# Kernel tuning notes

Measured on AMD Instinct MI355X. Metric: run time of the kernel, lower is better.

The kernel has to match this reference:

```python
import jax, jax.numpy as jnp
import numpy as np

D_MODEL = 1024
NUM_HEADS = 16

def _dense_params(key, d_in, d_out):
    kw, _ = jax.random.split(key)
    # flax default: lecun_normal kernel, zeros bias
    W = jax.random.normal(kw, (d_in, d_out), dtype=jnp.float32) / np.sqrt(d_in)
    b = jnp.zeros((d_out,), dtype=jnp.float32)
    return W, b

def setup_inputs() -> dict:
    key = jax.random.key(0)
    ks = jax.random.split(key, 8)
    B, Tx, Tc = 2, 2048, 2048
    x = jax.random.normal(ks[0], (B, Tx, D_MODEL), dtype=jnp.float32)
    context = jax.random.normal(ks[1], (B, Tc, D_MODEL), dtype=jnp.float32)
    Wq, bq = _dense_params(ks[2], D_MODEL, D_MODEL)
    Wks, bks = _dense_params(ks[3], D_MODEL, D_MODEL)
    Wvs, bvs = _dense_params(ks[4], D_MODEL, D_MODEL)
    Wkc, bkc = _dense_params(ks[5], D_MODEL, D_MODEL)
    Wvc, bvc = _dense_params(ks[6], D_MODEL, D_MODEL)
    Wo, bo = _dense_params(ks[7], D_MODEL, D_MODEL)
    return {"x": x, "context": context,
            "Wq": Wq, "bq": bq, "Wks": Wks, "bks": bks, "Wvs": Wvs, "bvs": bvs,
            "Wkc": Wkc, "bkc": bkc, "Wvc": Wvc, "bvc": bvc, "Wo": Wo, "bo": bo}

def _split_heads(t, H):
    B, T, C = t.shape
    return t.reshape(B, T, H, C // H).transpose(0, 2, 1, 3)  # [B,H,T,hd]

def reference(x, context, Wq, bq, Wks, bks, Wvs, bvs, Wkc, bkc, Wvc, bvc, Wo, bo):
    H = NUM_HEADS
    head_dim = D_MODEL // H
    q = x @ Wq + bq
    k = jnp.concatenate([x @ Wks + bks, context @ Wkc + bkc], axis=1)
    v = jnp.concatenate([x @ Wvs + bvs, context @ Wvc + bvc], axis=1)
    q = _split_heads(q, H)  # [B,H,Tq,hd]
    k = _split_heads(k, H)  # [B,H,Tk,hd]
    v = _split_heads(v, H)
    attn = jnp.einsum('bhqd,bhkd->bhqk', q, k) / jnp.sqrt(jnp.float32(head_dim))
    attn = jax.nn.softmax(attn, axis=-1)
    out = jnp.einsum('bhqk,bhkd->bhqd', attn, v)
    B, _, Tq, _ = out.shape
    out = out.transpose(0, 2, 1, 3).reshape(B, Tq, D_MODEL)
    return out @ Wo + bo
```

## Files before the change

### kernel.cpp

```cpp
#include <hip/hip_runtime.h>
#include <hip/hip_bf16.h>
#include <math.h>


typedef _Float16 f16;
typedef _Float16 f16x8 __attribute__((ext_vector_type(8)));
typedef _Float16 f16x4v __attribute__((ext_vector_type(4)));
typedef _Float16 f16x2 __attribute__((ext_vector_type(2)));
typedef float    f32x4 __attribute__((ext_vector_type(4)));
typedef float    f32x16 __attribute__((ext_vector_type(16)));
typedef unsigned u32x4v __attribute__((ext_vector_type(4)));

#define MFMA_F16(a, b, c)  __builtin_amdgcn_mfma_f32_16x16x32_f16((a), (b), (c), 0, 0, 0)
#define MFMA32_F16(a, b, c) __builtin_amdgcn_mfma_f32_32x32x16_f16((a), (b), (c), 0, 0, 0)

#define QSCALE 0.18033688011112042f

__device__ __forceinline__ void glds16(const f16* g, f16* l) {
    __builtin_amdgcn_global_load_lds(
        (const __attribute__((address_space(1))) void*)g,
        (__attribute__((address_space(3))) void*)l, 16, 0, 0);
}

__device__ __forceinline__ unsigned pk16(float a, float b) {
    f16x2 t = { (f16)a, (f16)b };
    return __builtin_bit_cast(unsigned, t);
}

__global__ __launch_bounds__(256) void prep(
    const float4* __restrict__ x, const float4* __restrict__ ctx,
    f16x4v* __restrict__ xb, f16x4v* __restrict__ cb,
    const float* __restrict__ W0, const float* __restrict__ W1,
    const float* __restrict__ W2, const float* __restrict__ W3,
    const float* __restrict__ W4, const float* __restrict__ W5,
    f16* __restrict__ wt)
{
    if (blockIdx.x < 8192) {
        const int n4 = (2 * 2048 * 1024) / 4;
        int i = blockIdx.x * 256 + threadIdx.x;
        float4 v;
        f16x4v* dst;
        if (i < n4) { v = x[i];        dst = xb + i; }
        else        { v = ctx[i - n4]; dst = cb + (i - n4); }
        f16x4v h = { (f16)v.x, (f16)v.y, (f16)v.z, (f16)v.w };
        *dst = h;
        return;
    }
    const int idx = blockIdx.x - 8192;
    const int z = idx >> 10, rem = idx & 1023;
    const float* Ws[6] = { W0, W1, W2, W3, W4, W5 };
    const float* W = Ws[z];
    f16* Wt = wt + (size_t)z * (1024 * 1024);

    __shared__ float tile[32][33];
    const int tx = threadIdx.x & 31, ty = threadIdx.x >> 5;
    const int n0 = (rem & 31) * 32, k0 = (rem >> 5) * 32;

#pragma unroll
    for (int i = 0; i < 4; ++i) {
        int r = i * 8 + ty;
        tile[r][tx] = W[(size_t)(k0 + r) * 1024 + n0 + tx];
    }
    __syncthreads();
#pragma unroll
    for (int i = 0; i < 4; ++i) {
        int r = i * 8 + ty;
        Wt[(size_t)(n0 + r) * 1024 + k0 + tx] = (f16)tile[tx][r];
    }
}

#define GEMM_PROLOGUE(BN)                                                     \
    const int m0 = blockIdx.x * 128, n0 = blockIdx.y * (BN);                  \
    const int tid = threadIdx.x;                                              \
    const int w = tid >> 6, lane = tid & 63, quad = lane >> 4, l15 = lane & 15;\
    const int wm = (w >> 1) * 64, wn = (w & 1) * ((BN) / 2);                  \
    const int qsw = (quad ^ ((l15 >> 1) & 3)) * 8;                            \
    int gA[2], gB[(BN) / 64];                                                 \
    _Pragma("unroll")                                                         \
    for (int p = 0; p < 2; ++p) {                                             \
        int s = tid + p * 256;                                                \
        int r = (s >> 2) & 127, c = (s & 3) ^ ((s >> 3) & 3);                 \
        gA[p] = (m0 + r) * 1024 + c * 8;                                      \
    }                                                                         \
    _Pragma("unroll")                                                         \
    for (int p = 0; p < (BN) / 64; ++p) {                                     \
        int s = tid + p * 256;                                                \
        int r = (s >> 2) & ((BN) - 1), c = (s & 3) ^ ((s >> 3) & 3);          \
        gB[p] = (n0 + r) * 1024 + c * 8;                                      \
    }

#define GEMM_STAGE_TO(BN, buf, koff)                                          \
    _Pragma("unroll")                                                         \
    for (int p = 0; p < 2; ++p)                                               \
        glds16(&A[gA[p] + (koff)], &As[buf][(p * 256 + w * 64) * 8]);         \
    _Pragma("unroll")                                                         \
    for (int p = 0; p < (BN) / 64; ++p)                                       \
        glds16(&Bt[gB[p] + (koff)], &Bs[buf][(p * 256 + w * 64) * 8]);

__global__ __launch_bounds__(256) void proj_gemm(
    const f16* __restrict__ xb, const f16* __restrict__ cb,
    const f16* __restrict__ wt,
    const float* __restrict__ bq, const float* __restrict__ bks,
    const float* __restrict__ bkc, const float* __restrict__ bvs,
    const float* __restrict__ bvc,
    f16* __restrict__ qbuf, f16* __restrict__ kbuf, f16* __restrict__ vbuf)
{
    __shared__ alignas(16) f16 As[2][128 * 32];
    __shared__ alignas(16) f16 Bs[2][128 * 32];

    const int z = blockIdx.z;
    const f16* A = (z == 0 || z == 1 || z == 3) ? xb : cb;
    const int wslot = (z == 0) ? 0 : (z == 1) ? 1 : (z == 2) ? 3 : (z == 3) ? 2 : 4;
    const f16* Bt = wt + (size_t)wslot * 1048576;
    const float* bias = (z == 0) ? bq : (z == 1) ? bks : (z == 2) ? bkc
                        : (z == 3) ? bvs : bvc;
    const int roff = (z == 2 || z == 4) ? 2048 : 0;

    GEMM_PROLOGUE(128)
    f32x4 acc[4][4] = {};

    GEMM_STAGE_TO(128, 0, 0)

    for (int k0 = 0; k0 < 1024; k0 += 32) {
        const int cur = (k0 >> 5) & 1;
        __syncthreads();
        if (k0 + 32 < 1024) {
            GEMM_STAGE_TO(128, cur ^ 1, k0 + 32)
        }
        f16x8 a[4], b[4];
#pragma unroll
        for (int i = 0; i < 4; ++i)
            a[i] = *(const f16x8*)&As[cur][(wm + i * 16 + l15) * 32 + qsw];
#pragma unroll
        for (int i = 0; i < 4; ++i)
            b[i] = *(const f16x8*)&Bs[cur][(wn + i * 16 + l15) * 32 + qsw];
#pragma unroll
        for (int mi = 0; mi < 4; ++mi)
#pragma unroll
            for (int ni = 0; ni < 4; ++ni)
                acc[mi][ni] = MFMA_F16(a[mi], b[ni], acc[mi][ni]);
    }

#pragma unroll
    for (int mi = 0; mi < 4; ++mi) {
#pragma unroll
        for (int r = 0; r < 4; ++r) {
            int row = m0 + wm + mi * 16 + quad * 4 + r;
            int b_ = row >> 11, tok = row & 2047;
#pragma unroll
            for (int ni = 0; ni < 4; ++ni) {
                int col = n0 + wn + ni * 16 + l15;
                float v = acc[mi][ni][r] + bias[col];
                int bh = b_ * 16 + (col >> 6);
                int tg = roff + tok;
                if (z == 0) {
                    qbuf[((size_t)bh * 2048 + tok) * 64 + (col & 63)] = (f16)(v * QSCALE);
                } else if (z <= 2) {
                    kbuf[(size_t)bh * 262144 + (size_t)(tg >> 6) * 4096
                         + (size_t)((col >> 5) & 1) * 2048 + (tg & 63) * 32 + (col & 31)] = (f16)v;
                } else {
                    vbuf[(size_t)bh * 262144 + (size_t)tg * 64 + (col & 63)] = (f16)v;
                }
            }
        }
    }
}

__global__ __launch_bounds__(256) void transpose_v(
    const f16* __restrict__ vbuf, f16* __restrict__ vt)
{
    const int t = threadIdx.x;
    const int mt = t >> 3, md = t & 7;
    const int tok0 = blockIdx.x * 256 + mt * 8;
    const int z = blockIdx.y;
    f16x8 in[8];
#pragma unroll
    for (int i = 0; i < 8; ++i)
        in[i] = *(const f16x8*)&vbuf[((size_t)z * 4096 + tok0 + i) * 64 + md * 8];
    f16x8 ov[8];
#pragma unroll
    for (int j = 0; j < 8; ++j)
#pragma unroll
        for (int i = 0; i < 8; ++i) ov[j][i] = in[i][j];
    const int kt = tok0 >> 6, kks = (tok0 >> 5) & 1, kko = tok0 & 31;
#pragma unroll
    for (int j = 0; j < 8; ++j)
        *(f16x8*)&vt[(size_t)z * 262144 + (size_t)kt * 4096 + kks * 2048
                     + (md * 8 + j) * 32 + kko] = ov[j];
}

__global__ __launch_bounds__(256, 4) void attn_kernel(
    const f16* __restrict__ q, const f16* __restrict__ kb,
    const f16* __restrict__ vtb, f16* __restrict__ osplit,
    float* __restrict__ lsplit)
{
    __shared__ alignas(16) f16 K_lds[2][4096];
    __shared__ alignas(16) f16 V_lds[2][4096];

    const int tid = threadIdx.x;
    const int w = tid >> 6, lane = tid & 63;
    const int l31 = lane & 31, h = lane >> 5;
    const int bh = blockIdx.x, qt = blockIdx.y, sp = blockIdx.z;
    const int qbase = qt * 128;

    f16x8 qa[4];
    {
        const size_t qrow = ((size_t)bh * 2048 + qbase + w * 32 + l31) * 64;
#pragma unroll
        for (int kc = 0; kc < 4; ++kc)
            qa[kc] = *(const f16x8*)&q[qrow + kc * 16 + h * 8];
    }

    f32x16 o_acc[2] = {};
    float l_part = 0.f;

    const f16* ktile = kb + (size_t)bh * 262144 + (size_t)sp * 131072;
    const f16* vtile = vtb + (size_t)bh * 262144 + (size_t)sp * 131072;

    const int sco = ((tid >> 2) * 4 + ((tid & 3) ^ ((tid >> 3) & 3))) * 8;
    const int ksw = (l31 >> 1) & 3;
    const int wslot = w * 512;

    glds16(ktile + sco,        &K_lds[0][wslot]);
    glds16(ktile + 2048 + sco, &K_lds[0][2048 + wslot]);
    glds16(vtile + sco,        &V_lds[0][wslot]);
    glds16(vtile + 2048 + sco, &V_lds[0][2048 + wslot]);

    for (int kt = 0; kt < 32; ++kt) {
        const int cur = kt & 1;
        const f16* Kc = K_lds[cur];
        const f16* Vc = V_lds[cur];

        __syncthreads();

        if (kt != 31) {
            ktile += 4096; vtile += 4096;
            glds16(ktile + sco,        &K_lds[cur ^ 1][wslot]);
            glds16(ktile + 2048 + sco, &K_lds[cur ^ 1][2048 + wslot]);
            glds16(vtile + sco,        &V_lds[cur ^ 1][wslot]);
            glds16(vtile + 2048 + sco, &V_lds[cur ^ 1][2048 + wslot]);
        }

#pragma unroll
        for (int mt = 0; mt < 2; ++mt) {
            f32x16 s = {};
            __builtin_amdgcn_s_setprio(1);
#pragma unroll
            for (int kc = 0; kc < 4; ++kc) {
                f16x8 ka = *(const f16x8*)&Kc[(kc >> 1) * 2048
                             + (mt * 32 + l31) * 32
                             + ((((kc & 1) * 2 + h) ^ ksw)) * 8];
                s = MFMA32_F16(ka, qa[kc], s);
            }
            __builtin_amdgcn_s_setprio(0);

            float pe[16];
#pragma unroll
            for (int i = 0; i < 16; ++i) pe[i] = __builtin_amdgcn_exp2f(s[i]);

            {
                float t0 = (pe[0] + pe[1]) + (pe[2] + pe[3]);
                float t1 = (pe[4] + pe[5]) + (pe[6] + pe[7]);
                float t2 = (pe[8] + pe[9]) + (pe[10] + pe[11]);
                float t3 = (pe[12] + pe[13]) + (pe[14] + pe[15]);
                l_part += (t0 + t1) + (t2 + t3);
            }

#pragma unroll
            for (int c = 0; c < 2; ++c) {
                const int cb = c * 8;
                unsigned X0 = pk16(pe[cb + 0], pe[cb + 1]);
                unsigned X1 = pk16(pe[cb + 2], pe[cb + 3]);
                unsigned Y0 = pk16(pe[cb + 4], pe[cb + 5]);
                unsigned Y1 = pk16(pe[cb + 6], pe[cb + 7]);
                auto r0 = __builtin_amdgcn_permlane32_swap(X0, Y0, false, false);
                auto r1 = __builtin_amdgcn_permlane32_swap(X1, Y1, false, false);
                u32x4v pw;
                pw[0] = r0[0]; pw[1] = r1[0]; pw[2] = r0[1]; pw[3] = r1[1];
                f16x8 pfrag = __builtin_bit_cast(f16x8, pw);

                const int kchunk = mt * 2 + c;
                __builtin_amdgcn_s_setprio(1);
#pragma unroll
                for (int db = 0; db < 2; ++db) {
                    f16x8 va = *(const f16x8*)&Vc[(kchunk >> 1) * 2048
                                 + (db * 32 + l31) * 32
                                 + (((((kchunk & 1) * 2 + h)) ^ ksw)) * 8];
                    o_acc[db] = MFMA32_F16(va, pfrag, o_acc[db]);
                }
                __builtin_amdgcn_s_setprio(0);
            }
        }
    }

    float lf = l_part + __shfl_xor(l_part, 32, 64);
    float inv = 1.0f / lf;
    const int row = w * 32 + l31;
    const size_t sb = (size_t)(sp * 32 + bh) * 2048 + qbase;
    if (h == 0) lsplit[sb + row] = lf;
    const size_t obase = (sb + row) * 64;
#pragma unroll
    for (int db = 0; db < 2; ++db) {
#pragma unroll
        for (int g = 0; g < 4; ++g) {
            f16x4v ov;
#pragma unroll
            for (int i = 0; i < 4; ++i)
                ov[i] = (f16)(o_acc[db][g * 4 + i] * inv);
            *(f16x4v*)&osplit[obase + db * 32 + g * 8 + h * 4] = ov;
        }
    }
}

__global__ __launch_bounds__(256) void combine(
    const f16* __restrict__ osplit, const float* __restrict__ lsplit,
    f16* __restrict__ abuf)
{
    int idx = blockIdx.x * 256 + threadIdx.x;
    int d8 = idx & 7;
    int row = (idx >> 3) & 2047;
    int bh = idx >> 14;
    int b = bh >> 4, h = bh & 15;
    size_t base1 = ((size_t)bh * 2048 + row) * 64 + d8 * 8;
    size_t base2 = ((size_t)(32 + bh) * 2048 + row) * 64 + d8 * 8;
    float l1 = lsplit[bh * 2048 + row];
    float l2 = lsplit[65536 + bh * 2048 + row];
    float inv = 1.0f / (l1 + l2);
    float w1 = l1 * inv, w2 = l2 * inv;
    f16x8 a = *(const f16x8*)&osplit[base1];
    f16x8 c = *(const f16x8*)&osplit[base2];
    f16x8 out;
#pragma unroll
    for (int j = 0; j < 8; ++j)
        out[j] = (f16)(w1 * (float)a[j] + w2 * (float)c[j]);
    *(f16x8*)&abuf[((size_t)(b * 2048 + row)) * 1024 + h * 64 + d8 * 8] = out;
}

__global__ __launch_bounds__(256) void out_gemm(
    const f16* __restrict__ abuf, const f16* __restrict__ wt5,
    const float* __restrict__ bo, float* __restrict__ out)
{
    __shared__ alignas(16) f16 As[2][128 * 32];
    __shared__ alignas(16) f16 Bs[2][64 * 32];

    const f16* A = abuf;
    const f16* Bt = wt5;

    GEMM_PROLOGUE(64)
    f32x4 acc[4][2] = {};

    GEMM_STAGE_TO(64, 0, 0)

    for (int k0 = 0; k0 < 1024; k0 += 32) {
        const int cur = (k0 >> 5) & 1;
        __syncthreads();
        if (k0 + 32 < 1024) {
            GEMM_STAGE_TO(64, cur ^ 1, k0 + 32)
        }
        f16x8 a[4], b[2];
#pragma unroll
        for (int i = 0; i < 4; ++i)
            a[i] = *(const f16x8*)&As[cur][(wm + i * 16 + l15) * 32 + qsw];
#pragma unroll
        for (int i = 0; i < 2; ++i)
            b[i] = *(const f16x8*)&Bs[cur][(wn + i * 16 + l15) * 32 + qsw];
#pragma unroll
        for (int mi = 0; mi < 4; ++mi)
#pragma unroll
            for (int ni = 0; ni < 2; ++ni)
                acc[mi][ni] = MFMA_F16(a[mi], b[ni], acc[mi][ni]);
    }

#pragma unroll
    for (int mi = 0; mi < 4; ++mi) {
#pragma unroll
        for (int r = 0; r < 4; ++r) {
            int row = m0 + wm + mi * 16 + quad * 4 + r;
#pragma unroll
            for (int ni = 0; ni < 2; ++ni) {
                int col = n0 + wn + ni * 16 + l15;
                out[(size_t)row * 1024 + col] = acc[mi][ni][r] + bo[col];
            }
        }
    }
}

extern "C" void kernel_launch(void* const* d_in, const int* in_sizes, int n_in,
                              void* d_out, int out_size, void* d_ws, size_t ws_size,
                              hipStream_t stream)
{
    (void)in_sizes; (void)n_in; (void)out_size; (void)ws_size;

    const float* x    = (const float*)d_in[0];
    const float* ctx  = (const float*)d_in[1];
    const float* Wq   = (const float*)d_in[2];  const float* bq  = (const float*)d_in[3];
    const float* Wks  = (const float*)d_in[4];  const float* bks = (const float*)d_in[5];
    const float* Wvs  = (const float*)d_in[6];  const float* bvs = (const float*)d_in[7];
    const float* Wkc  = (const float*)d_in[8];  const float* bkc = (const float*)d_in[9];
    const float* Wvc  = (const float*)d_in[10]; const float* bvc = (const float*)d_in[11];
    const float* Wo   = (const float*)d_in[12]; const float* bo  = (const float*)d_in[13];

    char* ws = (char*)d_ws;
    f16*   xb     = (f16*)(ws + 0);
    f16*   cb     = (f16*)(ws + 8388608);
    f16*   vt     = (f16*)(ws + 0);
    f16*   wt     = (f16*)(ws + 16777216);
    float* lsplit = (float*)(ws + 16777216);
    f16*   qbuf   = (f16*)(ws + 29360128);
    f16*   kbuf   = (f16*)(ws + 37748736);
    f16*   vbuf   = (f16*)(ws + 54525952);
    f16*   osplit = (f16*)(ws + 54525952);
    f16*   abuf   = (f16*)(ws + 71303168);

    prep<<<14336, 256, 0, stream>>>((const float4*)x, (const float4*)ctx,
                                    (f16x4v*)xb, (f16x4v*)cb,
                                    Wq, Wks, Wvs, Wkc, Wvc, Wo, wt);

    proj_gemm<<<dim3(32, 8, 5), 256, 0, stream>>>(
        xb, cb, wt, bq, bks, bkc, bvs, bvc, qbuf, kbuf, vbuf);

    transpose_v<<<dim3(16, 32), 256, 0, stream>>>(vbuf, vt);

    attn_kernel<<<dim3(32, 16, 2), 256, 0, stream>>>(qbuf, kbuf, vt, osplit, lsplit);

    combine<<<2048, 256, 0, stream>>>(osplit, lsplit, abuf);

    out_gemm<<<dim3(32, 16), 256, 0, stream>>>(abuf, wt + 5 * 1048576, bo, (float*)d_out);
}
```

Baseline: 307.3 us.

## Triple-buffer GEMM LDS staging with explicit vmcnt waits

Both projection and output GEMMs move from double to triple buffering of LDS tiles. Two stages are prefetched up front, and each iteration waits only for the oldest stage with a partial s_waitcnt vmcnt before issuing a raw s_barrier. This keeps a second global-to-LDS load in flight while compute proceeds, hiding load latency better. The cost is 50% more LDS per block, which may lower occupancy, and it relies on hand-counted outstanding-load numbers being correct.

```diff
diff --git a/kernel.cpp b/kernel.cpp
--- a/kernel.cpp
+++ b/kernel.cpp
@@ -105,8 +105,8 @@
     const float* __restrict__ bvc,
     f16* __restrict__ qbuf, f16* __restrict__ kbuf, f16* __restrict__ vbuf)
 {
-    __shared__ alignas(16) f16 As[2][128 * 32];
-    __shared__ alignas(16) f16 Bs[2][128 * 32];
+    __shared__ alignas(16) f16 As[3][128 * 32];
+    __shared__ alignas(16) f16 Bs[3][128 * 32];
 
     const int z = blockIdx.z;
     const f16* A = (z == 0 || z == 1 || z == 3) ? xb : cb;
@@ -120,20 +120,24 @@
     f32x4 acc[4][4] = {};
 
     GEMM_STAGE_TO(128, 0, 0)
-
-    for (int k0 = 0; k0 < 1024; k0 += 32) {
-        const int cur = (k0 >> 5) & 1;
-        __syncthreads();
-        if (k0 + 32 < 1024) {
-            GEMM_STAGE_TO(128, cur ^ 1, k0 + 32)
-        }
+    GEMM_STAGE_TO(128, 1, 32)
+
+    for (int it = 0; it < 32; ++it) {
+        if (it < 31) { asm volatile("s_waitcnt vmcnt(4)" ::: "memory"); }
+        else         { asm volatile("s_waitcnt vmcnt(0)" ::: "memory"); }
+        __builtin_amdgcn_s_barrier();
+        if (it + 2 < 32) {
+            GEMM_STAGE_TO(128, (it + 2) % 3, (it + 2) * 32)
+        }
+        const f16* Asc = As[it % 3];
+        const f16* Bsc = Bs[it % 3];
         f16x8 a[4], b[4];
 #pragma unroll
         for (int i = 0; i < 4; ++i)
-            a[i] = *(const f16x8*)&As[cur][(wm + i * 16 + l15) * 32 + qsw];
+            a[i] = *(const f16x8*)&Asc[(wm + i * 16 + l15) * 32 + qsw];
 #pragma unroll
         for (int i = 0; i < 4; ++i)
-            b[i] = *(const f16x8*)&Bs[cur][(wn + i * 16 + l15) * 32 + qsw];
+            b[i] = *(const f16x8*)&Bsc[(wn + i * 16 + l15) * 32 + qsw];
 #pragma unroll
         for (int mi = 0; mi < 4; ++mi)
 #pragma unroll
@@ -340,8 +344,8 @@
     const f16* __restrict__ abuf, const f16* __restrict__ wt5,
     const float* __restrict__ bo, float* __restrict__ out)
 {
-    __shared__ alignas(16) f16 As[2][128 * 32];
-    __shared__ alignas(16) f16 Bs[2][64 * 32];
+    __shared__ alignas(16) f16 As[3][128 * 32];
+    __shared__ alignas(16) f16 Bs[3][64 * 32];
 
     const f16* A = abuf;
     const f16* Bt = wt5;
@@ -350,20 +354,24 @@
     f32x4 acc[4][2] = {};
 
     GEMM_STAGE_TO(64, 0, 0)
-
-    for (int k0 = 0; k0 < 1024; k0 += 32) {
-        const int cur = (k0 >> 5) & 1;
-        __syncthreads();
-        if (k0 + 32 < 1024) {
-            GEMM_STAGE_TO(64, cur ^ 1, k0 + 32)
-        }
+    GEMM_STAGE_TO(64, 1, 32)
+
+    for (int it = 0; it < 32; ++it) {
+        if (it < 31) { asm volatile("s_waitcnt vmcnt(3)" ::: "memory"); }
+        else         { asm volatile("s_waitcnt vmcnt(0)" ::: "memory"); }
+        __builtin_amdgcn_s_barrier();
+        if (it + 2 < 32) {
+            GEMM_STAGE_TO(64, (it + 2) % 3, (it + 2) * 32)
+        }
+        const f16* Asc = As[it % 3];
+        const f16* Bsc = Bs[it % 3];
         f16x8 a[4], b[2];
 #pragma unroll
         for (int i = 0; i < 4; ++i)
-            a[i] = *(const f16x8*)&As[cur][(wm + i * 16 + l15) * 32 + qsw];
+            a[i] = *(const f16x8*)&Asc[(wm + i * 16 + l15) * 32 + qsw];
 #pragma unroll
         for (int i = 0; i < 2; ++i)
-            b[i] = *(const f16x8*)&Bs[cur][(wn + i * 16 + l15) * 32 + qsw];
+            b[i] = *(const f16x8*)&Bsc[(wn + i * 16 + l15) * 32 + qsw];
 #pragma unroll
         for (int mi = 0; mi < 4; ++mi)
 #pragma unroll
```

New measurement: 301.3 us. About the same (-2.0%).
